# Performance work log

Measured on AMD Instinct MI355X. Metric: run time of the kernel, lower is better.

Reference implementation:

```python
import jax, jax.numpy as jnp
import numpy as np

N = 20000    # num nodes
E = 320000   # num edges (also rows of edge_type, SPN line-graph style)
F = 64       # num_features
HID = 64     # hidden_channels
HEADS = 4    # gatv2_heads
NC = 2       # num_classes
PH = 128     # proxy hidden size
SLOPE = 0.2  # PyG GATv2 leaky_relu negative slope


def gatv2(feat, src, dst, wl, wr, att, b, num_nodes, concat):
    # GATv2Conv (PyG semantics, add_self_loops=True, dropout off in eval)
    H, C = att.shape
    xl = (feat @ wl).reshape(-1, H, C)
    xr = (feat @ wr).reshape(-1, H, C)
    loops = jnp.arange(num_nodes, dtype=src.dtype)
    s = jnp.concatenate([src, loops])
    d = jnp.concatenate([dst, loops])
    e = jax.nn.leaky_relu(xl[s] + xr[d], SLOPE)            # [E', H, C]
    logits = jnp.einsum('ehc,hc->eh', e, att)              # [E', H]
    m = jax.ops.segment_max(logits, d, num_segments=num_nodes)
    p = jnp.exp(logits - m[d])
    z = jax.ops.segment_sum(p, d, num_segments=num_nodes)
    alpha = p / z[d]                                       # segment softmax
    out = jax.ops.segment_sum(xl[s] * alpha[:, :, None], d, num_segments=num_nodes)
    out = out.reshape(num_nodes, H * C) if concat else out.mean(axis=1)
    return out + b


def setup_inputs():
    key = jax.random.key(0)
    ks = iter(jax.random.split(key, 32))
    def rn(shape, scale=0.1):
        return jax.random.normal(next(ks), shape, dtype=jnp.float32) * scale
    return {
        'x': rn((N, F), 1.0),
        'edge_type': rn((E, F), 1.0),
        'edge_index': jax.random.randint(next(ks), (2, E), 0, N, dtype=jnp.int32),
        'n1_wl': rn((F, HEADS * HID)), 'n1_wr': rn((F, HEADS * HID)),
        'n1_att': rn((HEADS, HID)), 'n1_b': jnp.zeros((HEADS * HID,), jnp.float32),
        'n2_wl': rn((HEADS * HID, HID)), 'n2_wr': rn((HEADS * HID, HID)),
        'n2_att': rn((1, HID)), 'n2_b': jnp.zeros((HID,), jnp.float32),
        'e1_wl': rn((F, HEADS * HID)), 'e1_wr': rn((F, HEADS * HID)),
        'e1_att': rn((HEADS, HID)), 'e1_b': jnp.zeros((HEADS * HID,), jnp.float32),
        'e2_wl': rn((HEADS * HID, HID)), 'e2_wr': rn((HEADS * HID, HID)),
        'e2_att': rn((1, HID)), 'e2_b': jnp.zeros((HID,), jnp.float32),
        'crf_wu': rn((HID, NC)), 'crf_bu': jnp.zeros((NC,), jnp.float32),
        'crf_wp': rn((HID, NC)),
        'px_w1': rn((HID, PH)), 'px_b1': jnp.zeros((PH,), jnp.float32),
        'px_w2': rn((PH, NC)), 'px_b2': jnp.zeros((NC,), jnp.float32),
    }


def reference(x, edge_type, edge_index, n1_wl, n1_wr, n1_att, n1_b, n2_wl, n2_wr, n2_att, n2_b,
              e1_wl, e1_wr, e1_att, e1_b, e2_wl, e2_wr, e2_att, e2_b,
              crf_wu, crf_bu, crf_wp, px_w1, px_b1, px_w2, px_b2):
    src, dst = edge_index[0], edge_index[1]
    # node GNN: GATv2 -> ELU -> GATv2 (dropout = identity in eval)
    h = jax.nn.elu(gatv2(x, src, dst, n1_wl, n1_wr, n1_att, n1_b, N, True))
    node_repr = gatv2(h, src, dst, n2_wl, n2_wr, n2_att, n2_b, N, False)
    # edge GNN over edge features (E rows, same edge_index, per source code)
    g = jax.nn.elu(gatv2(edge_type, src, dst, e1_wl, e1_wr, e1_att, e1_b, E, True))
    edge_repr = gatv2(g, src, dst, e2_wl, e2_wr, e2_att, e2_b, E, False)
    # CRF head: unary potentials + pairwise messages scattered to dst nodes
    unary = node_repr @ crf_wu + crf_bu
    msg = jax.ops.segment_sum(edge_repr @ crf_wp, dst, num_segments=N)
    crf_out = jax.nn.log_softmax(unary + msg, axis=-1)
    # MLP proxy head
    ph = jax.nn.relu(node_repr @ px_w1 + px_b1)
    proxy_out = ph @ px_w2 + px_b2
    return crf_out, proxy_out
```

## Files before the change

### kernel.cpp

```cpp
#include <hip/hip_runtime.h>
#include <cstddef>
#include <cstdint>

#define N_NODES 20000
#define N_EDGES 320000

typedef __attribute__((ext_vector_type(8))) short bf8_t;
typedef __attribute__((ext_vector_type(4))) float f4_t;
typedef __attribute__((ext_vector_type(2))) float f2_t;
typedef unsigned short bfu;
typedef __attribute__((ext_vector_type(4))) unsigned short us4_t;
typedef __attribute__((ext_vector_type(8))) unsigned short us8_t;

__device__ __forceinline__ short f2bf(float f) {
  unsigned u = __float_as_uint(f);
  u += 0x7fff + ((u >> 16) & 1);
  return (short)(u >> 16);
}
__device__ __forceinline__ f2_t leaky2(f2_t t) {
  f2_t zero = {0.f, 0.f};
  f2_t mx = __builtin_elementwise_max(t, zero);
  f2_t mn = __builtin_elementwise_min(t, zero);
  return mn * 0.2f + mx;
}
__device__ __forceinline__ void bf8_to_f2x4(us8_t xu, f2_t o[4]) {
  union { us8_t v; unsigned u[4]; } c; c.v = xu;
  #pragma unroll
  for (int j = 0; j < 4; ++j) {
    unsigned d = c.u[j];
    f2_t t;
    t.x = __uint_as_float(d << 16);
    t.y = __uint_as_float(d & 0xffff0000u);
    o[j] = t;
  }
}

__global__ void count_deg_kernel(const int* __restrict__ dst, int* __restrict__ deg, int e_cnt) {
  int e = blockIdx.x * blockDim.x + threadIdx.x;
  if (e < e_cnt) atomicAdd(&deg[dst[e]], 1);
}

__global__ __launch_bounds__(1024) void scan_kernel(
    const int* __restrict__ deg, int* __restrict__ rowptr,
    int* __restrict__ cursor, int n) {
  __shared__ int sdata[1024];
  const int CH = (n + 1023) / 1024;
  int tid = threadIdx.x;
  int base = tid * CH;
  int loc[20];
  int s = 0;
  for (int j = 0; j < CH; ++j) {
    int idx = base + j;
    int v = (idx < n) ? deg[idx] : 0;
    loc[j] = s;
    s += v;
  }
  sdata[tid] = s;
  __syncthreads();
  for (int off = 1; off < 1024; off <<= 1) {
    int t = (tid >= off) ? sdata[tid - off] : 0;
    __syncthreads();
    sdata[tid] += t;
    __syncthreads();
  }
  int excl = sdata[tid] - s;
  for (int j = 0; j < CH; ++j) {
    int idx = base + j;
    if (idx < n) { int val = excl + loc[j]; rowptr[idx] = val; cursor[idx] = val; }
  }
  if (tid == 0) rowptr[n] = sdata[1023];
}

__global__ void fill_csr_kernel(const int* __restrict__ src, const int* __restrict__ dst,
                                int* __restrict__ cursor, int* __restrict__ csr_src,
                                int* __restrict__ csr_eid, int e_cnt) {
  int e = blockIdx.x * blockDim.x + threadIdx.x;
  if (e < e_cnt) {
    int pos = atomicAdd(&cursor[dst[e]], 1);
    csr_src[pos] = src[e];
    csr_eid[pos] = e;
  }
}

__global__ void prep_all_kernel(
    const float* __restrict__ n1l, const float* __restrict__ n1r,
    const float* __restrict__ e1l, const float* __restrict__ e1r,
    const float* __restrict__ n2l, const float* __restrict__ n2r,
    const float* __restrict__ e2l, const float* __restrict__ e2r,
    const float* __restrict__ b2, const float* __restrict__ wp,
    short* __restrict__ t_n1l, short* __restrict__ t_n1r,
    short* __restrict__ t_e1l, short* __restrict__ t_e1r,
    short* __restrict__ t_n2l, short* __restrict__ t_n2r,
    short* __restrict__ t_e2l, short* __restrict__ t_e2r,
    float* __restrict__ wct, float* __restrict__ pc)
{
  int i = blockIdx.x * blockDim.x + threadIdx.x;
  int seg = i >> 14;
  int j = i & 16383;
  if (seg < 4) {
    const float* srcs[4] = {n1l, n1r, e1l, e1r};
    short* dsts[4] = {t_n1l, t_n1r, t_e1l, t_e1r};
    int n = j >> 6, k = j & 63;
    dsts[seg][n * 64 + k] = f2bf(srcs[seg][k * 256 + n]);
  } else if (seg < 8) {
    const float* srcs[4] = {n2l, n2r, e2l, e2r};
    short* dsts[4] = {t_n2l, t_n2r, t_e2l, t_e2r};
    int n = j >> 8, k = j & 255;
    dsts[seg - 4][n * 256 + k] = f2bf(srcs[seg - 4][k * 64 + n]);
  } else if (seg == 8) {
    if (j < 512) {
      int jj = j & 1;
      int k  = j >> 1;
      float s = 0.f;
      for (int c = 0; c < 64; ++c) s = fmaf(e2l[k * 64 + c], wp[c * 2 + jj], s);
      wct[jj * 256 + k] = s;
    } else if (j < 514) {
      int jj = j - 512;
      float s = 0.f;
      for (int c = 0; c < 64; ++c) s = fmaf(b2[c], wp[c * 2 + jj], s);
      pc[jj] = s;
    }
  }
}

template<int K>
__global__ __launch_bounds__(128) void mfma_proj2_kernel(
    const float* __restrict__ A0,
    const short* __restrict__ Wtl0, const short* __restrict__ Wtr0,
    bfu* __restrict__ xl0, float* __restrict__ xr0,
    const float* __restrict__ A1,
    const short* __restrict__ Wtl1, const short* __restrict__ Wtr1,
    bfu* __restrict__ xl1, float* __restrict__ xr1,
    int M, int nslices)
{
  constexpr int KC = K / 32;
  int tid = threadIdx.x;
  int w = tid >> 6, lane = tid & 63, quad = lane >> 4, l15 = lane & 15;
  int row_base = (int)blockIdx.x * 64 + w * 32;
  int y = (int)blockIdx.y;
  int z = (int)blockIdx.z;
  const float* A = z ? A1 : A0;
  bool is_l = y < nslices;
  const short* Wt = z ? (is_l ? Wtl1 : Wtr1) : (is_l ? Wtl0 : Wtr0);
  bfu* xl = z ? xl1 : xl0;
  float* xr = z ? xr1 : xr0;
  int cb = (is_l ? y : y - nslices) * 64;
  int STR = nslices * 64;

  bf8_t a[2][KC];
  #pragma unroll
  for (int rt = 0; rt < 2; ++rt) {
    int r = row_base + rt * 16 + l15;
    int rc = r < M ? r : M - 1;
    const float* ap = A + (size_t)rc * K + quad * 8;
    #pragma unroll
    for (int kc = 0; kc < KC; ++kc) {
      float4 v0 = *(const float4*)(ap + kc * 32);
      float4 v1 = *(const float4*)(ap + kc * 32 + 4);
      bf8_t f;
      f[0] = f2bf(v0.x); f[1] = f2bf(v0.y); f[2] = f2bf(v0.z); f[3] = f2bf(v0.w);
      f[4] = f2bf(v1.x); f[5] = f2bf(v1.y); f[6] = f2bf(v1.z); f[7] = f2bf(v1.w);
      a[rt][kc] = f;
    }
  }

  #pragma unroll
  for (int nt = 0; nt < 4; ++nt) {
    f4_t acc0 = {0.f, 0.f, 0.f, 0.f};
    f4_t acc1 = {0.f, 0.f, 0.f, 0.f};
    const short* wb = Wt + (size_t)(cb + nt * 16 + l15) * K + quad * 8;
    #pragma unroll
    for (int kc = 0; kc < KC; ++kc) {
      bf8_t wf = *(const bf8_t*)(wb + kc * 32);
      acc0 = __builtin_amdgcn_mfma_f32_16x16x32_bf16(wf, a[0][kc], acc0, 0, 0, 0);
      acc1 = __builtin_amdgcn_mfma_f32_16x16x32_bf16(wf, a[1][kc], acc1, 0, 0, 0);
    }
    #pragma unroll
    for (int rt = 0; rt < 2; ++rt) {
      f4_t acc = rt == 0 ? acc0 : acc1;
      int row = row_base + rt * 16 + l15;
      if (row >= M) continue;
      int col = cb + nt * 16 + quad * 4;
      if (is_l) {
        us4_t pk;
        pk[0] = (bfu)f2bf(acc[0]); pk[1] = (bfu)f2bf(acc[1]);
        pk[2] = (bfu)f2bf(acc[2]); pk[3] = (bfu)f2bf(acc[3]);
        *(us4_t*)&xl[(size_t)row * STR + col] = pk;
      } else {
        *(float4*)&xr[(size_t)row * STR + col] = make_float4(acc[0], acc[1], acc[2], acc[3]);
      }
    }
  }
}

template<int KIN>
__device__ __forceinline__ void gemm_body(
    const float* __restrict__ A, const float* __restrict__ W, int wld, int cb,
    int block_m, int M, float (&acc)[8][4],
    float (*As)[128 + 4], float (*Ws)[64 + 4])
{
  int tid = threadIdx.x;
  int tx = tid & 15;
  int ty = tid >> 4;
  #pragma unroll
  for (int i = 0; i < 8; ++i)
    #pragma unroll
    for (int j = 0; j < 4; ++j) acc[i][j] = 0.f;

  for (int k0 = 0; k0 < KIN; k0 += 16) {
    #pragma unroll
    for (int rep = 0; rep < 2; ++rep) {
      int ar = (tid >> 2) + rep * 64;
      int ak = (tid & 3) * 4;
      int gr = block_m + ar;
      float4 v = make_float4(0.f, 0.f, 0.f, 0.f);
      if (gr < M) v = *(const float4*)&A[(size_t)gr * KIN + k0 + ak];
      As[ak + 0][ar] = v.x; As[ak + 1][ar] = v.y;
      As[ak + 2][ar] = v.z; As[ak + 3][ar] = v.w;
    }
    {
      int wr = tid >> 4;
      int wc = (tid & 15) * 4;
      float4 v = *(const float4*)&W[(size_t)(k0 + wr) * wld + cb + wc];
      Ws[wr][wc + 0] = v.x; Ws[wr][wc + 1] = v.y;
      Ws[wr][wc + 2] = v.z; Ws[wr][wc + 3] = v.w;
    }
    __syncthreads();
    #pragma unroll
    for (int k = 0; k < 16; ++k) {
      float a[8], w[4];
      #pragma unroll
      for (int i = 0; i < 8; ++i) a[i] = As[k][ty * 8 + i];
      #pragma unroll
      for (int j = 0; j < 4; ++j) w[j] = Ws[k][tx * 4 + j];
      #pragma unroll
      for (int i = 0; i < 8; ++i)
        #pragma unroll
        for (int j = 0; j < 4; ++j) acc[i][j] = fmaf(a[i], w[j], acc[i][j]);
    }
    __syncthreads();
  }
}

template<int KIN, int MODE>
__global__ __launch_bounds__(256) void gemm64_kernel(
    const float* __restrict__ A, const float* __restrict__ W, int wld,
    const float* __restrict__ bias, float* __restrict__ out, int old, int M)
{
  __shared__ float As[16][128 + 4];
  __shared__ float Ws[16][64 + 4];
  float acc[8][4];
  int block_m = (int)blockIdx.x * 128;
  int cb = (int)blockIdx.y * 64;
  gemm_body<KIN>(A, W, wld, cb, block_m, M, acc, As, Ws);

  int tid = threadIdx.x;
  int tx = tid & 15, ty = tid >> 4;
  int gc = cb + tx * 4;
  #pragma unroll
  for (int i = 0; i < 8; ++i) {
    int gr = block_m + ty * 8 + i;
    if (gr >= M) continue;
    size_t idx = (size_t)gr * old + gc;
    float t0 = acc[i][0], t1 = acc[i][1], t2 = acc[i][2], t3 = acc[i][3];
    if (MODE == 3) {
      t0 = fmaxf(t0 + bias[gc + 0], 0.f);
      t1 = fmaxf(t1 + bias[gc + 1], 0.f);
      t2 = fmaxf(t2 + bias[gc + 2], 0.f);
      t3 = fmaxf(t3 + bias[gc + 3], 0.f);
    }
    *(float4*)&out[idx] = make_float4(t0, t1, t2, t3);
  }
}

template<bool ELU, int STR, bool FUSEP>
__global__ __launch_bounds__(STR == 256 ? 256 : 64) void gat_agg_v4(
    const bfu* __restrict__ xl0, const float* __restrict__ xr0,
    const float* __restrict__ att0, const float* __restrict__ bias0,
    float* __restrict__ out0, int old0,
    const bfu* __restrict__ xl1, const float* __restrict__ xr1,
    const float* __restrict__ att1, const float* __restrict__ bias1,
    float* __restrict__ out1, int old1,
    const int* __restrict__ rowptr, const int* __restrict__ csr_src,
    const float* __restrict__ wp, float* __restrict__ pbuf)
{
  int d = blockIdx.x;
  bool c1 = d >= N_NODES;
  if (c1) d -= N_NODES;
  const bfu* xl = c1 ? xl1 : xl0;
  const float* xr = c1 ? xr1 : xr0;
  const float* att = c1 ? att1 : att0;
  const float* bias = c1 ? bias1 : bias0;

  int tid = threadIdx.x;
  int h = tid >> 6;
  int lane = tid & 63;
  int egrp = lane >> 3;
  int cch  = lane & 7;
  int row0 = rowptr[d];
  int deg = rowptr[d + 1] - row0;
  int cbase = h * 64 + cch * 8;

  f2_t xr2[4], att2[4];
  {
    const float* xrp = xr + (size_t)d * STR + cbase;
    const float* atp = att + cbase;
    float4 a0 = *(const float4*)(xrp);
    float4 a1 = *(const float4*)(xrp + 4);
    xr2[0] = f2_t{a0.x, a0.y}; xr2[1] = f2_t{a0.z, a0.w};
    xr2[2] = f2_t{a1.x, a1.y}; xr2[3] = f2_t{a1.z, a1.w};
    float4 b0 = *(const float4*)(atp);
    float4 b1 = *(const float4*)(atp + 4);
    att2[0] = f2_t{b0.x, b0.y}; att2[1] = f2_t{b0.z, b0.w};
    att2[2] = f2_t{b1.x, b1.y}; att2[3] = f2_t{b1.z, b1.w};
  }

  float zloc;
  f2_t acc4[4];
  {
    us8_t xu = *(const us8_t*)&xl[(size_t)d * STR + cbase];
    f2_t xs[4];
    bf8_to_f2x4(xu, xs);
    f2_t p2 = {0.f, 0.f};
    #pragma unroll
    for (int j = 0; j < 4; ++j) p2 = p2 + leaky2(xs[j] + xr2[j]) * att2[j];
    float part = p2.x + p2.y;
    part += __shfl_xor(part, 1, 64);
    part += __shfl_xor(part, 2, 64);
    part += __shfl_xor(part, 4, 64);
    float w = __expf(part);
    float ws = (egrp == 0) ? w : 0.f;
    zloc = ws;
    f2_t ws2 = {ws, ws};
    #pragma unroll
    for (int j = 0; j < 4; ++j) acc4[j] = xs[j] * ws2;
  }

  for (int j = 0; j < deg; j += 8) {
    int idx = j + egrp;
    bool valid = idx < deg;
    int s = valid ? csr_src[row0 + idx] : d;
    us8_t xu = *(const us8_t*)&xl[(size_t)s * STR + cbase];
    f2_t xf[4];
    bf8_to_f2x4(xu, xf);
    f2_t p2 = {0.f, 0.f};
    #pragma unroll
    for (int i = 0; i < 4; ++i) p2 = p2 + leaky2(xf[i] + xr2[i]) * att2[i];
    float part = p2.x + p2.y;
    part += __shfl_xor(part, 1, 64);
    part += __shfl_xor(part, 2, 64);
    part += __shfl_xor(part, 4, 64);
    float w = valid ? __expf(part) : 0.f;
    zloc += w;
    f2_t w2 = {w, w};
    #pragma unroll
    for (int i = 0; i < 4; ++i) acc4[i] = acc4[i] + xf[i] * w2;
  }

  float a8[8];
  #pragma unroll
  for (int i = 0; i < 4; ++i) { a8[2 * i] = acc4[i].x; a8[2 * i + 1] = acc4[i].y; }
  #pragma unroll
  for (int off = 8; off < 64; off <<= 1) {
    zloc += __shfl_xor(zloc, off, 64);
    #pragma unroll
    for (int i = 0; i < 8; ++i) a8[i] += __shfl_xor(a8[i], off, 64);
  }

  float invz = 1.f / zloc;
  float o[8];
  #pragma unroll
  for (int i = 0; i < 8; ++i) {
    float val = a8[i] * invz + bias[cbase + i];
    if (ELU) val = val > 0.f ? val : __expf(val) - 1.f;
    o[i] = val;
  }

  if (FUSEP && c1) {
    float p0 = 0.f, p1 = 0.f;
    #pragma unroll
    for (int i = 0; i < 8; ++i) {
      float2 wv = *(const float2*)&wp[(cbase + i) * 2];
      p0 = fmaf(o[i], wv.x, p0);
      p1 = fmaf(o[i], wv.y, p1);
    }
    p0 += __shfl_xor(p0, 1, 64); p1 += __shfl_xor(p1, 1, 64);
    p0 += __shfl_xor(p0, 2, 64); p1 += __shfl_xor(p1, 2, 64);
    p0 += __shfl_xor(p0, 4, 64); p1 += __shfl_xor(p1, 4, 64);
    if (lane == 0) *(float2*)&pbuf[2 * d] = make_float2(p0, p1);
  } else if (egrp == 0) {
    float* out = c1 ? out1 : out0;
    int old = c1 ? old1 : old0;
    float* op = out + (size_t)d * old + cbase;
    *(float4*)(op)     = make_float4(o[0], o[1], o[2], o[3]);
    *(float4*)(op + 4) = make_float4(o[4], o[5], o[6], o[7]);
  }
}

__global__ __launch_bounds__(256) void chunk_fold_kernel(
    const float* __restrict__ A,
    const short* __restrict__ W1t,
    const float* __restrict__ b1,
    const float* __restrict__ WcT,
    const float* __restrict__ pc,
    float* __restrict__ pbufN,
    int Mtot)
{
  int tid = threadIdx.x;
  int w = tid >> 6;
  int lane = tid & 63;
  int quad = lane >> 4;
  int l15 = lane & 15;
  int row_base = (int)blockIdx.x * 256 + w * 64;

  bf8_t a1[4][2];
  #pragma unroll
  for (int rt = 0; rt < 4; ++rt) {
    int r = row_base + rt * 16 + l15;
    int rc = r < Mtot ? r : Mtot - 1;
    const float* ap = A + (size_t)rc * 64 + quad * 8;
    #pragma unroll
    for (int ks = 0; ks < 2; ++ks) {
      float4 v0 = *(const float4*)(ap + ks * 32);
      float4 v1 = *(const float4*)(ap + ks * 32 + 4);
      bf8_t f;
      f[0] = f2bf(v0.x); f[1] = f2bf(v0.y); f[2] = f2bf(v0.z); f[3] = f2bf(v0.w);
      f[4] = f2bf(v1.x); f[5] = f2bf(v1.y); f[6] = f2bf(v1.z); f[7] = f2bf(v1.w);
      a1[rt][ks] = f;
    }
  }

  float p0[4] = {0.f, 0.f, 0.f, 0.f};
  float p1[4] = {0.f, 0.f, 0.f, 0.f};

  #pragma unroll
  for (int cc = 0; cc < 4; ++cc) {
    #pragma unroll
    for (int nt = 0; nt < 4; ++nt) {
      const short* wb = W1t + (cc * 64 + nt * 16 + l15) * 64 + quad * 8;
      bf8_t w0 = *(const bf8_t*)(wb);
      bf8_t w1 = *(const bf8_t*)(wb + 32);
      f4_t g[4];
      #pragma unroll
      for (int rt = 0; rt < 4; ++rt) {
        f4_t z = {0.f, 0.f, 0.f, 0.f};
        z = __builtin_amdgcn_mfma_f32_16x16x32_bf16(w0, a1[rt][0], z, 0, 0, 0);
        z = __builtin_amdgcn_mfma_f32_16x16x32_bf16(w1, a1[rt][1], z, 0, 0, 0);
        g[rt] = z;
      }
      int cbase = cc * 64 + nt * 16 + quad * 4;
      f4_t b4  = *(const f4_t*)&b1[cbase];
      f4_t wc0 = *(const f4_t*)&WcT[cbase];
      f4_t wc1 = *(const f4_t*)&WcT[256 + cbase];
      #pragma unroll
      for (int rt = 0; rt < 4; ++rt) {
        #pragma unroll
        for (int r = 0; r < 4; ++r) {
          float v = g[rt][r] + b4[r];
          v = v > 0.f ? v : __expf(v) - 1.f;
          p0[rt] = fmaf(v, wc0[r], p0[rt]);
          p1[rt] = fmaf(v, wc1[r], p1[rt]);
        }
      }
    }
  }

  #pragma unroll
  for (int off = 16; off < 64; off <<= 1) {
    #pragma unroll
    for (int rt = 0; rt < 4; ++rt) {
      p0[rt] += __shfl_xor(p0[rt], off, 64);
      p1[rt] += __shfl_xor(p1[rt], off, 64);
    }
  }
  if (quad == 0) {
    float c0 = pc[0], c1 = pc[1];
    #pragma unroll
    for (int rt = 0; rt < 4; ++rt) {
      int row = row_base + rt * 16 + l15;
      if (row < Mtot)
        *(float2*)&pbufN[2 * row] = make_float2(p0[rt] + c0, p1[rt] + c1);
    }
  }
}

__global__ void head_kernel(const float* __restrict__ node_repr, const float* __restrict__ ph,
                            const int* __restrict__ rowptr, const int* __restrict__ csr_eid,
                            const float* __restrict__ pbuf, const float* __restrict__ wu,
                            const float* __restrict__ bu, const float* __restrict__ w2,
                            const float* __restrict__ b2, float* __restrict__ out, int n) {
  __shared__ float swu[128];
  __shared__ float sw2[256];
  int tid = threadIdx.x;
  if (tid < 128) swu[tid] = wu[tid];
  sw2[tid] = w2[tid];
  __syncthreads();
  int i = blockIdx.x * blockDim.x + tid;
  if (i >= n) return;
  float m0 = 0.f, m1 = 0.f;
  int r0 = rowptr[i], r1 = rowptr[i + 1];
  int jj = r0;
  for (; jj + 4 <= r1; jj += 4) {
    int e0 = csr_eid[jj + 0], e1 = csr_eid[jj + 1];
    int e2 = csr_eid[jj + 2], e3 = csr_eid[jj + 3];
    float2 q0 = *(const float2*)&pbuf[2 * e0];
    float2 q1 = *(const float2*)&pbuf[2 * e1];
    float2 q2 = *(const float2*)&pbuf[2 * e2];
    float2 q3 = *(const float2*)&pbuf[2 * e3];
    m0 += (q0.x + q1.x) + (q2.x + q3.x);
    m1 += (q0.y + q1.y) + (q2.y + q3.y);
  }
  for (; jj < r1; ++jj) {
    int e = csr_eid[jj];
    float2 q = *(const float2*)&pbuf[2 * e];
    m0 += q.x; m1 += q.y;
  }
  const float* nr = node_repr + (size_t)i * 64;
  float u0 = bu[0], u1 = bu[1];
  #pragma unroll
  for (int k = 0; k < 64; ++k) {
    float v = nr[k];
    u0 = fmaf(v, swu[2 * k + 0], u0);
    u1 = fmaf(v, swu[2 * k + 1], u1);
  }
  float v0 = u0 + m0;
  float v1 = u1 + m1;
  float mx = fmaxf(v0, v1);
  float lse = mx + logf(__expf(v0 - mx) + __expf(v1 - mx));
  out[2 * i + 0] = v0 - lse;
  out[2 * i + 1] = v1 - lse;
  const float* p = ph + (size_t)i * 128;
  float p0 = b2[0], p1 = b2[1];
  #pragma unroll
  for (int k = 0; k < 128; ++k) {
    float v = p[k];
    p0 = fmaf(v, sw2[2 * k + 0], p0);
    p1 = fmaf(v, sw2[2 * k + 1], p1);
  }
  out[2 * n + 2 * i + 0] = p0;
  out[2 * n + 2 * i + 1] = p1;
}

extern "C" void kernel_launch(void* const* d_in, const int* in_sizes, int n_in,
                              void* d_out, int out_size, void* d_ws, size_t ws_size,
                              hipStream_t stream) {
  const int N = N_NODES, E = N_EDGES;
  const float* x         = (const float*)d_in[0];
  const float* edge_type = (const float*)d_in[1];
  const int*   ei        = (const int*)d_in[2];
  const float* n1_wl  = (const float*)d_in[3];
  const float* n1_wr  = (const float*)d_in[4];
  const float* n1_att = (const float*)d_in[5];
  const float* n1_b   = (const float*)d_in[6];
  const float* n2_wl  = (const float*)d_in[7];
  const float* n2_wr  = (const float*)d_in[8];
  const float* n2_att = (const float*)d_in[9];
  const float* n2_b   = (const float*)d_in[10];
  const float* e1_wl  = (const float*)d_in[11];
  const float* e1_wr  = (const float*)d_in[12];
  const float* e1_att = (const float*)d_in[13];
  const float* e1_b   = (const float*)d_in[14];
  const float* e2_wl  = (const float*)d_in[15];
  const float* e2_wr  = (const float*)d_in[16];
  const float* e2_att = (const float*)d_in[17];
  const float* e2_b   = (const float*)d_in[18];
  const float* crf_wu = (const float*)d_in[19];
  const float* crf_bu = (const float*)d_in[20];
  const float* crf_wp = (const float*)d_in[21];
  const float* px_w1  = (const float*)d_in[22];
  const float* px_b1  = (const float*)d_in[23];
  const float* px_w2  = (const float*)d_in[24];
  const float* px_b2  = (const float*)d_in[25];
  float* out = (float*)d_out;
  const int* src = ei;
  const int* dst = ei + E;
  (void)in_sizes; (void)n_in; (void)out_size; (void)ws_size;

  char* ws = (char*)d_ws;
  size_t off = 0;
  auto alloc = [&](size_t bytes) -> void* {
    void* p = ws + off;
    off += (bytes + 255) & ~(size_t)255;
    return p;
  };
  bfu*   xl_n  = (bfu*)alloc((size_t)N * 256 * 2);
  float* xr_n  = (float*)alloc((size_t)N * 256 * 4);
  bfu*   xl_e  = (bfu*)alloc((size_t)N * 256 * 2);
  float* xr_e  = (float*)alloc((size_t)N * 256 * 4);
  float* h_n   = (float*)alloc((size_t)N * 256 * 4);
  float* g_e   = (float*)alloc((size_t)N * 256 * 4);
  bfu*   xl2_n = (bfu*)alloc((size_t)N * 64 * 2);
  float* xr2_n = (float*)alloc((size_t)N * 64 * 4);
  bfu*   xl2_e = (bfu*)alloc((size_t)N * 64 * 2);
  float* xr2_e = (float*)alloc((size_t)N * 64 * 4);
  float* B3    = (float*)alloc((size_t)N * 64 * 4);
  float* pbuf  = (float*)alloc((size_t)E * 2 * 4);
  float* ph    = (float*)(void*)xl_n;
  int* deg     = (int*)alloc((size_t)N * 4);
  int* rowptr  = (int*)alloc((size_t)(N + 1) * 4);
  int* cursor  = (int*)alloc((size_t)N * 4);
  int* csr_src = (int*)alloc((size_t)E * 4);
  int* csr_eid = (int*)alloc((size_t)E * 4);
  short* t_n1l = (short*)alloc((size_t)16384 * 2);
  short* t_n1r = (short*)alloc((size_t)16384 * 2);
  short* t_e1l = (short*)alloc((size_t)16384 * 2);
  short* t_e1r = (short*)alloc((size_t)16384 * 2);
  short* t_n2l = (short*)alloc((size_t)16384 * 2);
  short* t_n2r = (short*)alloc((size_t)16384 * 2);
  short* t_e2l = (short*)alloc((size_t)16384 * 2);
  short* t_e2r = (short*)alloc((size_t)16384 * 2);
  float* WcT   = (float*)alloc((size_t)2 * 256 * 4);
  float* pcv   = (float*)alloc((size_t)2 * 4);

  const int EB = (E + 255) / 256;
  const int NB = (N + 127) / 128;
  const int PB = (N + 63) / 64;
  const int Mhigh = E - N;
  const int CFB = (Mhigh + 255) / 256;

  hipMemsetAsync(deg, 0, (size_t)N * 4, stream);
  count_deg_kernel<<<EB, 256, 0, stream>>>(dst, deg, E);
  scan_kernel<<<1, 1024, 0, stream>>>(deg, rowptr, cursor, N);
  fill_csr_kernel<<<EB, 256, 0, stream>>>(src, dst, cursor, csr_src, csr_eid, E);
  prep_all_kernel<<<515, 256, 0, stream>>>(n1_wl, n1_wr, e1_wl, e1_wr,
                                           n2_wl, n2_wr, e2_wl, e2_wr,
                                           e2_b, crf_wp,
                                           t_n1l, t_n1r, t_e1l, t_e1r,
                                           t_n2l, t_n2r, t_e2l, t_e2r, WcT, pcv);

  mfma_proj2_kernel<64><<<dim3(PB, 8, 2), 128, 0, stream>>>(
      x, t_n1l, t_n1r, xl_n, xr_n,
      edge_type, t_e1l, t_e1r, xl_e, xr_e, N, 4);
  gat_agg_v4<true, 256, false><<<2 * N, 256, 0, stream>>>(
      xl_n, xr_n, n1_att, n1_b, h_n, 256,
      xl_e, xr_e, e1_att, e1_b, g_e, 256, rowptr, csr_src, nullptr, nullptr);

  mfma_proj2_kernel<256><<<dim3(PB, 2, 2), 128, 0, stream>>>(
      h_n, t_n2l, t_n2r, xl2_n, xr2_n,
      g_e, t_e2l, t_e2r, xl2_e, xr2_e, N, 1);
  gat_agg_v4<false, 64, true><<<2 * N, 64, 0, stream>>>(
      xl2_n, xr2_n, n2_att, n2_b, B3, 64,
      xl2_e, xr2_e, e2_att, e2_b, nullptr, 64, rowptr, csr_src, crf_wp, pbuf);

  chunk_fold_kernel<<<CFB, 256, 0, stream>>>(edge_type + (size_t)N * 64, t_e1l,
                                             e1_b, WcT, pcv, pbuf + 2 * (size_t)N, Mhigh);

  gemm64_kernel<64, 3><<<dim3(NB, 2), 256, 0, stream>>>(B3, px_w1, 128, px_b1, ph, 128, N);
  head_kernel<<<(N + 255) / 256, 256, 0, stream>>>(B3, ph, rowptr, csr_eid, pbuf,
                                                   crf_wu, crf_bu, px_w2, px_b2, out, N);
}
```

Before: 465.6 us.

## Remap GAT aggregation to one wave per node-head and prefetch neighbor gathers

Rewrites the GAT aggregation kernel so each 256-thread block covers four destination nodes for one head, with each wave handling one (node, head) pair. This replaces the old layouts of one block per node with four heads per wave, and 64-thread blocks for the single-head layer. The edge loop now software-pipelines its loads: it keeps the current gathered row, prefetches the next row and the index two chunks ahead, using clamped index loads. The goal is to hide gather latency and to keep blocks full for the second layer, at the cost of more registers and some redundant index loads.

After: 459.9 us. No clear change (-1.2%).

```diff
diff --git a/kernel.cpp b/kernel.cpp
--- a/kernel.cpp
+++ b/kernel.cpp
@@ -273,33 +273,40 @@
   }
 }
 
-template<bool ELU, int STR, bool FUSEP>
-__global__ __launch_bounds__(STR == 256 ? 256 : 64) void gat_agg_v4(
+template<int STR, bool ELU, bool FUSEP>
+__global__ __launch_bounds__(256) void gat_agg_v5(
     const bfu* __restrict__ xl0, const float* __restrict__ xr0,
     const float* __restrict__ att0, const float* __restrict__ bias0,
-    float* __restrict__ out0, int old0,
+    float* __restrict__ out0,
     const bfu* __restrict__ xl1, const float* __restrict__ xr1,
     const float* __restrict__ att1, const float* __restrict__ bias1,
-    float* __restrict__ out1, int old1,
+    float* __restrict__ out1,
     const int* __restrict__ rowptr, const int* __restrict__ csr_src,
     const float* __restrict__ wp, float* __restrict__ pbuf)
 {
-  int d = blockIdx.x;
-  bool c1 = d >= N_NODES;
-  if (c1) d -= N_NODES;
-  const bfu* xl = c1 ? xl1 : xl0;
-  const float* xr = c1 ? xr1 : xr0;
-  const float* att = c1 ? att1 : att0;
-  const float* bias = c1 ? bias1 : bias0;
-
+  constexpr int HEADS = STR / 64;
+  constexpr int GRP = N_NODES / 4;
   int tid = threadIdx.x;
-  int h = tid >> 6;
+  int w = tid >> 6;
   int lane = tid & 63;
   int egrp = lane >> 3;
   int cch  = lane & 7;
+
+  int bid = (int)blockIdx.x;
+  int per_chain = HEADS * GRP;
+  int chain = bid >= per_chain ? 1 : 0;
+  int r = bid - chain * per_chain;
+  int head = r / GRP;
+  int d = (r - head * GRP) * 4 + w;
+
+  const bfu* xl = chain ? xl1 : xl0;
+  const float* xr = chain ? xr1 : xr0;
+  const float* att = chain ? att1 : att0;
+  const float* bias = chain ? bias1 : bias0;
+
   int row0 = rowptr[d];
   int deg = rowptr[d + 1] - row0;
-  int cbase = h * 64 + cch * 8;
+  int cbase = head * 64 + cch * 8;
 
   f2_t xr2[4], att2[4];
   {
@@ -315,6 +322,14 @@
     att2[2] = f2_t{b1.x, b1.y}; att2[3] = f2_t{b1.z, b1.w};
   }
 
+  auto ld_idx = [&](int k) -> int {
+    int idx = k * 8 + egrp;
+    int cl = idx < deg ? idx : (deg > 0 ? deg - 1 : 0);
+    int pos = deg > 0 ? row0 + cl : 0;
+    int sv = csr_src[pos];
+    return idx < deg ? sv : d;
+  };
+
   float zloc;
   f2_t acc4[4];
   {
@@ -328,21 +343,24 @@
     part += __shfl_xor(part, 1, 64);
     part += __shfl_xor(part, 2, 64);
     part += __shfl_xor(part, 4, 64);
-    float w = __expf(part);
-    float ws = (egrp == 0) ? w : 0.f;
+    float wgt = __expf(part);
+    float ws = (egrp == 0) ? wgt : 0.f;
     zloc = ws;
     f2_t ws2 = {ws, ws};
     #pragma unroll
     for (int j = 0; j < 4; ++j) acc4[j] = xs[j] * ws2;
   }
 
-  for (int j = 0; j < deg; j += 8) {
-    int idx = j + egrp;
-    bool valid = idx < deg;
-    int s = valid ? csr_src[row0 + idx] : d;
-    us8_t xu = *(const us8_t*)&xl[(size_t)s * STR + cbase];
+  int C = (deg + 7) >> 3;
+  int s_cur = ld_idx(0);
+  us8_t xu_cur = *(const us8_t*)&xl[(size_t)s_cur * STR + cbase];
+  int s_nxt = ld_idx(1);
+  for (int k = 0; k < C; ++k) {
+    us8_t xu_nxt = *(const us8_t*)&xl[(size_t)s_nxt * STR + cbase];
+    int s_n2 = ld_idx(k + 2);
+    bool valid = (k * 8 + egrp) < deg;
     f2_t xf[4];
-    bf8_to_f2x4(xu, xf);
+    bf8_to_f2x4(xu_cur, xf);
     f2_t p2 = {0.f, 0.f};
     #pragma unroll
     for (int i = 0; i < 4; ++i) p2 = p2 + leaky2(xf[i] + xr2[i]) * att2[i];
@@ -350,11 +368,13 @@
     part += __shfl_xor(part, 1, 64);
     part += __shfl_xor(part, 2, 64);
     part += __shfl_xor(part, 4, 64);
-    float w = valid ? __expf(part) : 0.f;
-    zloc += w;
-    f2_t w2 = {w, w};
+    float wgt = valid ? __expf(part) : 0.f;
+    zloc += wgt;
+    f2_t w2 = {wgt, wgt};
     #pragma unroll
     for (int i = 0; i < 4; ++i) acc4[i] = acc4[i] + xf[i] * w2;
+    xu_cur = xu_nxt;
+    s_nxt = s_n2;
   }
 
   float a8[8];
@@ -376,7 +396,7 @@
     o[i] = val;
   }
 
-  if (FUSEP && c1) {
+  if (FUSEP && chain) {
     float p0 = 0.f, p1 = 0.f;
     #pragma unroll
     for (int i = 0; i < 8; ++i) {
@@ -389,9 +409,8 @@
     p0 += __shfl_xor(p0, 4, 64); p1 += __shfl_xor(p1, 4, 64);
     if (lane == 0) *(float2*)&pbuf[2 * d] = make_float2(p0, p1);
   } else if (egrp == 0) {
-    float* out = c1 ? out1 : out0;
-    int old = c1 ? old1 : old0;
-    float* op = out + (size_t)d * old + cbase;
+    float* out = chain ? out1 : out0;
+    float* op = out + (size_t)d * STR + cbase;
     *(float4*)(op)     = make_float4(o[0], o[1], o[2], o[3]);
     *(float4*)(op + 4) = make_float4(o[4], o[5], o[6], o[7]);
   }
@@ -617,6 +636,7 @@
   const int PB = (N + 63) / 64;
   const int Mhigh = E - N;
   const int CFB = (Mhigh + 255) / 256;
+  const int GRP = N / 4;
 
   hipMemsetAsync(deg, 0, (size_t)N * 4, stream);
   count_deg_kernel<<<EB, 256, 0, stream>>>(dst, deg, E);
@@ -631,16 +651,16 @@
   mfma_proj2_kernel<64><<<dim3(PB, 8, 2), 128, 0, stream>>>(
       x, t_n1l, t_n1r, xl_n, xr_n,
       edge_type, t_e1l, t_e1r, xl_e, xr_e, N, 4);
-  gat_agg_v4<true, 256, false><<<2 * N, 256, 0, stream>>>(
-      xl_n, xr_n, n1_att, n1_b, h_n, 256,
-      xl_e, xr_e, e1_att, e1_b, g_e, 256, rowptr, csr_src, nullptr, nullptr);
+  gat_agg_v5<256, true, false><<<2 * 4 * GRP, 256, 0, stream>>>(
+      xl_n, xr_n, n1_att, n1_b, h_n,
+      xl_e, xr_e, e1_att, e1_b, g_e, rowptr, csr_src, nullptr, nullptr);
 
   mfma_proj2_kernel<256><<<dim3(PB, 2, 2), 128, 0, stream>>>(
       h_n, t_n2l, t_n2r, xl2_n, xr2_n,
       g_e, t_e2l, t_e2r, xl2_e, xr2_e, N, 1);
-  gat_agg_v4<false, 64, true><<<2 * N, 64, 0, stream>>>(
-      xl2_n, xr2_n, n2_att, n2_b, B3, 64,
-      xl2_e, xr2_e, e2_att, e2_b, nullptr, 64, rowptr, csr_src, crf_wp, pbuf);
+  gat_agg_v5<64, false, true><<<2 * GRP, 256, 0, stream>>>(
+      xl2_n, xr2_n, n2_att, n2_b, B3,
+      xl2_e, xr2_e, e2_att, e2_b, nullptr, rowptr, csr_src, crf_wp, pbuf);
 
   chunk_fold_kernel<<<CFB, 256, 0, stream>>>(edge_type + (size_t)N * 64, t_e1l,
                                              e1_b, WcT, pcv, pbuf + 2 * (size_t)N, Mhigh);
```
